# Optimization experiments

Hardware: AMD Instinct MI355X
Metric: run time of the kernel (lower is better)

## Reference

```python
import jax, jax.numpy as jnp
import numpy as np
from jax import lax

MAX_INT = 10000.0
V, T0, E, H = 100000, 20, 256, 256
T = T0 + 2          # tagset_size + 2 (start = T-2, stop = T-1)
B, S = 32, 512
H2 = H // 2


def setup_inputs() -> dict:
    key = jax.random.key(0)
    ks = jax.random.split(key, 18)
    sd = 0.08
    trans = jax.random.normal(ks[0], (T, T), jnp.float32)
    trans = trans.at[-2, :].set(-MAX_INT).at[:, -1].set(-MAX_INT)
    return {
        "X": jax.random.randint(ks[1], (B, S), 0, V, jnp.int64),
        "Y": jax.random.randint(ks[2], (B, S), 0, T0, jnp.int64),
        "emb": jax.random.normal(ks[3], (V, E), jnp.float32) * sd,
        "Wih_f": jax.random.normal(ks[4], (4 * H2, E), jnp.float32) * sd,
        "Whh_f": jax.random.normal(ks[5], (4 * H2, H2), jnp.float32) * sd,
        "bih_f": jax.random.normal(ks[6], (4 * H2,), jnp.float32) * sd,
        "bhh_f": jax.random.normal(ks[7], (4 * H2,), jnp.float32) * sd,
        "Wih_b": jax.random.normal(ks[8], (4 * H2, E), jnp.float32) * sd,
        "Whh_b": jax.random.normal(ks[9], (4 * H2, H2), jnp.float32) * sd,
        "bih_b": jax.random.normal(ks[10], (4 * H2,), jnp.float32) * sd,
        "bhh_b": jax.random.normal(ks[11], (4 * H2,), jnp.float32) * sd,
        "fcW": jax.random.normal(ks[12], (T, H), jnp.float32) * sd,
        "fcb": jax.random.normal(ks[13], (T,), jnp.float32) * sd,
        "trans": trans,
        # original draws random (h0, c0) of shape (2, seq_len, H//2) each call
        "h0": jax.random.normal(ks[14], (2, S, H2), jnp.float32),
        "c0": jax.random.normal(ks[15], (2, S, H2), jnp.float32),
    }


def _lstm_dir(x, h0, c0, Wih, Whh, bih, bhh, reverse):
    # x: [B, S, E]; scans over axis 0 (as torch LSTM with batch_first=False does here)
    def step(carry, xt):
        h, c = carry
        g = xt @ Wih.T + bih + h @ Whh.T + bhh          # [S, 4*H2]
        i, f, gg, o = jnp.split(g, 4, axis=-1)
        c2 = jax.nn.sigmoid(f) * c + jax.nn.sigmoid(i) * jnp.tanh(gg)
        h2 = jax.nn.sigmoid(o) * jnp.tanh(c2)
        return (h2, c2), h2
    xs = x[::-1] if reverse else x
    _, hs = lax.scan(step, (h0, c0), xs)
    return hs[::-1] if reverse else hs                  # [B, S, H2]


def _feats(X, emb, Wih_f, Whh_f, bih_f, bhh_f, Wih_b, Whh_b, bih_b, bhh_b,
           fcW, fcb, h0, c0):
    e = emb[X]                                           # [B, S, E]
    hf = _lstm_dir(e, h0[0], c0[0], Wih_f, Whh_f, bih_f, bhh_f, False)
    hb = _lstm_dir(e, h0[1], c0[1], Wih_b, Whh_b, bih_b, bhh_b, True)
    lstm_out = jnp.concatenate([hf, hb], axis=-1)        # [B, S, H]
    return lstm_out @ fcW.T + fcb                        # [B, S, T]


def _crf_loss(feats, Y, trans):
    # forward algorithm (log partition), vectorized over batch
    alpha0 = jnp.full((B, T), -MAX_INT, feats.dtype).at[:, -2].set(0.0)

    def step(alpha, feat_t):                             # feat_t: [B, T]
        # alpha_new[b, next] = LSE_prev(alpha[b,prev] + trans[next,prev]) + feat[b,next]
        new = jax.nn.logsumexp(alpha[:, None, :] + trans[None, :, :], axis=2) + feat_t
        return new, None

    alpha, _ = lax.scan(step, alpha0, jnp.swapaxes(feats, 0, 1))
    forward_score = jax.nn.logsumexp(alpha + trans[-1][None, :], axis=1).mean()

    # gold score
    start = jnp.full((B, 1), T - 2, Y.dtype)
    tags = jnp.concatenate([start, Y], axis=1)           # [B, S+1]
    emit = jnp.take_along_axis(feats, Y[..., None], axis=2)[..., 0].sum(axis=1)
    trans_sc = trans[tags[:, 1:], tags[:, :-1]].sum(axis=1) + trans[-1, tags[:, -1]]
    gold_score = (emit + trans_sc).mean()
    return forward_score - gold_score


def reference(X, Y, emb, Wih_f, Whh_f, bih_f, bhh_f, Wih_b, Whh_b, bih_b, bhh_b,
              fcW, fcb, trans, h0, c0):
    feats = _feats(X, emb, Wih_f, Whh_f, bih_f, bhh_f, Wih_b, Whh_b, bih_b, bhh_b,
                   fcW, fcb, h0, c0)
    score = _crf_loss(feats, Y, trans)
    return score, Y
```

## Files before the change

kernel.cpp:

```cpp
#include <hip/hip_runtime.h>
#include <hip/hip_bf16.h>
#include <stdint.h>

typedef __attribute__((ext_vector_type(8))) short short8;
typedef __attribute__((ext_vector_type(4))) float f32x4;
typedef __attribute__((ext_vector_type(4))) unsigned short ushort4v;
typedef __attribute__((ext_vector_type(4))) unsigned int uint4v;

#define NB 32
#define NS 512
#define NE 256
#define NH2 128
#define NG 512
#define NT 22

__device__ __forceinline__ unsigned short f2bf(float f) {
    union { float f; unsigned u; } v; v.f = f;
    unsigned r = v.u + 0x7fffu + ((v.u >> 16) & 1u);
    return (unsigned short)(r >> 16);
}
__device__ __forceinline__ float bf2f(unsigned short b) {
    union { unsigned u; float f; } v; v.u = ((unsigned)b) << 16;
    return v.f;
}
__device__ __forceinline__ unsigned cvt_pk_bf16(float a, float b) {
    unsigned r;
    asm("v_cvt_pk_bf16_f32 %0, %1, %2" : "=v"(r) : "v"(a), "v"(b));
    return r;
}
__device__ __forceinline__ void wg_barrier() {
    __builtin_amdgcn_sched_barrier(0);
    asm volatile("s_waitcnt lgkmcnt(0)" ::: "memory");
    __builtin_amdgcn_s_barrier();
    __builtin_amdgcn_sched_barrier(0);
}
#define GL16(gsrc, ldst)                                                              \
    __builtin_amdgcn_global_load_lds(                                                 \
        (const __attribute__((address_space(1))) unsigned int*)(gsrc),                \
        (__attribute__((address_space(3))) unsigned int*)(ldst), 16, 0, 0)

__global__ void k_pre(const int* X, const float* emb, const int* Y,
                      const float* Wih_f, const float* Wih_b,
                      const float* Whh_f, const float* Whh_b, const float* fcW,
                      unsigned short* ebf, unsigned short* Wb_ih,
                      unsigned short* Wb_hh, unsigned short* fcpad, float* out)
{
    int idx = blockIdx.x * blockDim.x + threadIdx.x;
    const int nEmb = NB * NS * 64;
    if (idx < nEmb) {
        int r = idx >> 6, lane = idx & 63;
        int xr = X[r];
        f32x4 v = *(const f32x4*)(emb + (size_t)xr * NE + lane * 4);
        ushort4v o;
        o[0] = f2bf(v[0]); o[1] = f2bf(v[1]); o[2] = f2bf(v[2]); o[3] = f2bf(v[3]);
        *(ushort4v*)(ebf + (size_t)r * NE + lane * 4) = o;
        return;
    }
    int j = idx - nEmb;
    const int n1 = 2 * NG * NE;
    const int n2 = 2 * NG * NH2;
    const int n3 = 2 * 32 * NH2;
    const int n4 = NB * NS;
    if (j < n1) {
        const float* src = (j < NG * NE) ? Wih_f : Wih_b;
        Wb_ih[j] = f2bf(src[j % (NG * NE)]);
    } else if (j < n1 + n2) {
        int i2 = j - n1;
        const float* src = (i2 < NG * NH2) ? Whh_f : Whh_b;
        Wb_hh[i2] = f2bf(src[i2 % (NG * NH2)]);
    } else if (j < n1 + n2 + n3) {
        int i3 = j - n1 - n2;
        int d = i3 / (32 * NH2);
        int jj = (i3 / NH2) % 32;
        int k = i3 % NH2;
        fcpad[i3] = (jj < NT) ? f2bf(fcW[jj * 256 + d * NH2 + k]) : (unsigned short)0;
    } else if (j < n1 + n2 + n3 + n4) {
        int i4 = j - n1 - n2 - n3;
        out[1 + i4] = (float)Y[i4];
    }
}

__launch_bounds__(256)
__global__ void k_xproj(const unsigned short* ebf, const unsigned short* Wb_ih,
                        const float* bih_f, const float* bhh_f,
                        const float* bih_b, const float* bhh_b,
                        unsigned short* Xp)
{
    __shared__ __align__(16) unsigned short Atile[2][128 * 64];
    __shared__ __align__(16) unsigned short Btile[2][128 * 64];
    int dir = blockIdx.z;
    int r0 = blockIdx.x * 128;
    int g0 = blockIdx.y * 128;
    int tid = threadIdx.x;
    int w = tid >> 6, lane = tid & 63;
    int wr = w >> 1, wc = w & 1;
    int lrow = lane & 15, kg = lane >> 4;
    int srow8 = lane >> 3, schunk = lane & 7;
    const float* bih = dir ? bih_b : bih_f;
    const float* bhh = dir ? bhh_b : bhh_f;
    const unsigned short* Bsrc = Wb_ih + ((size_t)dir * NG + g0) * NE;
    const unsigned short* Asrc = ebf + (size_t)r0 * NE;

#define STAGE(bufi, ks)                                                                \
    do {                                                                               \
        int k0_ = (ks) * 64;                                                           \
        _Pragma("unroll")                                                              \
        for (int i_ = 0; i_ < 4; ++i_) {                                               \
            int rr_ = (w * 4 + i_) * 8 + srow8;                                        \
            GL16(Asrc + (size_t)rr_ * NE + k0_ + schunk * 8, &Atile[bufi][(w * 4 + i_) * 512]); \
            GL16(Bsrc + (size_t)rr_ * NE + k0_ + schunk * 8, &Btile[bufi][(w * 4 + i_) * 512]); \
        }                                                                              \
    } while (0)

    STAGE(0, 0);
    f32x4 acc[4][4] = {};
#pragma unroll
    for (int ks = 0; ks < 4; ++ks) {
        const int cur = ks & 1;
        if (ks < 3) {
            STAGE(cur ^ 1, ks + 1);
            asm volatile("s_waitcnt vmcnt(8)" ::: "memory");
        } else {
            asm volatile("s_waitcnt vmcnt(0)" ::: "memory");
        }
        __builtin_amdgcn_sched_barrier(0);
        __builtin_amdgcn_s_barrier();
        __builtin_amdgcn_sched_barrier(0);
        short8 a[4][2], b[4][2];
#pragma unroll
        for (int mi = 0; mi < 4; ++mi)
#pragma unroll
            for (int kk = 0; kk < 2; ++kk)
                a[mi][kk] = *(const short8*)&Atile[cur][(wr * 64 + mi * 16 + lrow) * 64 + kk * 32 + kg * 8];
#pragma unroll
        for (int ni = 0; ni < 4; ++ni)
#pragma unroll
            for (int kk = 0; kk < 2; ++kk)
                b[ni][kk] = *(const short8*)&Btile[cur][(wc * 64 + ni * 16 + lrow) * 64 + kk * 32 + kg * 8];
#pragma unroll
        for (int mi = 0; mi < 4; ++mi)
#pragma unroll
            for (int ni = 0; ni < 4; ++ni)
#pragma unroll
                for (int kk = 0; kk < 2; ++kk)
                    acc[mi][ni] = __builtin_amdgcn_mfma_f32_16x16x32_bf16(a[mi][kk], b[ni][kk], acc[mi][ni], 0, 0, 0);
        asm volatile("s_waitcnt lgkmcnt(0)" ::: "memory");
        __builtin_amdgcn_sched_barrier(0);
        __builtin_amdgcn_s_barrier();
        __builtin_amdgcn_sched_barrier(0);
    }
#undef STAGE

#pragma unroll
    for (int ni = 0; ni < 4; ++ni) {
        int g = g0 + wc * 64 + ni * 16 + lrow;
        float bias = bih[g] + bhh[g];
#pragma unroll
        for (int mi = 0; mi < 4; ++mi) {
            int r = r0 + wr * 64 + mi * 16 + kg * 4;
            int t = r >> 9;
            int s = r & 511;
            int sb = s >> 4;
            unsigned short* dst = Xp + ((((size_t)dir * 32 + sb) * 32 + t) << 13) + g * 16 + (s & 15);
            unsigned o0 = f2bf(acc[mi][ni][0] + bias);
            unsigned o1 = f2bf(acc[mi][ni][1] + bias);
            unsigned o2 = f2bf(acc[mi][ni][2] + bias);
            unsigned o3 = f2bf(acc[mi][ni][3] + bias);
            uint2 pk; pk.x = o0 | (o1 << 16); pk.y = o2 | (o3 << 16);
            *(uint2*)dst = pk;
        }
    }
}

__launch_bounds__(512, 2)
__global__ void k_lstm(const unsigned short* Wb_hh, const unsigned short* fcpad,
                       const unsigned short* Xp, const float* h0, const float* c0,
                       unsigned short* featsP)
{
    __shared__ unsigned short h_lds[2][16 * 136];
    __shared__ unsigned short featsL[512 * 24];
    int dir = blockIdx.x >> 5;
    int sb = blockIdx.x & 31;
    int s0 = sb * 16;
    int tid = threadIdx.x;
    int w = tid >> 6, lane = tid & 63;
    int lrow = lane & 15, kg = lane >> 4;

    short8 bfr[4][4];
#pragma unroll
    for (int q = 0; q < 4; ++q) {
        const unsigned short* p = Wb_hh + ((size_t)dir * NG + (q * 128 + w * 16 + lrow)) * NH2 + kg * 8;
#pragma unroll
        for (int kf = 0; kf < 4; ++kf)
            bfr[q][kf] = *(const short8*)(p + kf * 32);
    }
    short8 fcfr[4];
    if (w < 2) {
        const unsigned short* p = fcpad + ((size_t)dir * 32 + (w * 16 + lrow)) * NH2 + kg * 8;
#pragma unroll
        for (int kf = 0; kf < 4; ++kf)
            fcfr[kf] = *(const short8*)(p + kf * 32);
    }

    float c[4], ho[4];
#pragma unroll
    for (int i = 0; i < 4; ++i)
        c[i] = c0[((size_t)dir * NS + s0 + kg * 4 + i) * NH2 + w * 16 + lrow];
    {
        int sl = tid >> 5, hq = tid & 31;
        f32x4 hv = *(const f32x4*)(h0 + ((size_t)dir * NS + s0 + sl) * NH2 + hq * 4);
        ushort4v hb; hb[0] = f2bf(hv[0]); hb[1] = f2bf(hv[1]); hb[2] = f2bf(hv[2]); hb[3] = f2bf(hv[3]);
        *(ushort4v*)&h_lds[0][sl * 136 + hq * 4] = hb;
    }

    const unsigned short* xbase = Xp + (((size_t)dir * 32 + sb) * 32) * 8192;
    int xoff0 = (w * 16 + lrow) * 16 + kg * 4;
    ushort4v xA[4], xB[4];
#pragma unroll
    for (int q = 0; q < 4; ++q)
        xA[q] = *(const ushort4v*)(xbase + (size_t)(dir ? 31 : 0) * 8192 + xoff0 + q * 2048);
#pragma unroll
    for (int q = 0; q < 4; ++q)
        xB[q] = *(const ushort4v*)(xbase + (size_t)(dir ? 30 : 1) * 8192 + xoff0 + q * 2048);
    __syncthreads();

#define LSTM_STEP(T, XV, PR, PW)                                                       \
    {                                                                                  \
        short8 afr[4];                                                                 \
        _Pragma("unroll")                                                              \
        for (int kf = 0; kf < 4; ++kf)                                                 \
            afr[kf] = *(const short8*)&h_lds[PR][lrow * 136 + kf * 32 + kg * 8];       \
        f32x4 accA[4], accB[4];                                                        \
        _Pragma("unroll")                                                              \
        for (int q = 0; q < 4; ++q) {                                                  \
            f32x4 ci_;                                                                 \
            ci_[0] = bf2f(XV[q][0]); ci_[1] = bf2f(XV[q][1]);                          \
            ci_[2] = bf2f(XV[q][2]); ci_[3] = bf2f(XV[q][3]);                          \
            accA[q] = __builtin_amdgcn_mfma_f32_16x16x32_bf16(afr[0], bfr[q][0], ci_, 0, 0, 0); \
            f32x4 z_ = {};                                                             \
            accB[q] = __builtin_amdgcn_mfma_f32_16x16x32_bf16(afr[2], bfr[q][2], z_, 0, 0, 0);  \
        }                                                                              \
        _Pragma("unroll")                                                              \
        for (int q = 0; q < 4; ++q) {                                                  \
            accA[q] = __builtin_amdgcn_mfma_f32_16x16x32_bf16(afr[1], bfr[q][1], accA[q], 0, 0, 0); \
            accB[q] = __builtin_amdgcn_mfma_f32_16x16x32_bf16(afr[3], bfr[q][3], accB[q], 0, 0, 0); \
        }                                                                              \
        if (w < 2 && (T) > 0) {                    \
            int txp_ = dir ? 32 - (T) : (T) - 1;                                       \
            f32x4 fa_ = {};                                                            \
            _Pragma("unroll")                                                          \
            for (int kf = 0; kf < 4; ++kf)                                             \
                fa_ = __builtin_amdgcn_mfma_f32_16x16x32_bf16(afr[kf], fcfr[kf], fa_, 0, 0, 0); \
            int tag_ = w * 16 + lrow;                                                  \
            if (tag_ < NT) {                                                           \
                unsigned r01_ = cvt_pk_bf16(fa_[0], fa_[1]);                           \
                unsigned r23_ = cvt_pk_bf16(fa_[2], fa_[3]);                           \
                int rb_ = (txp_ * 16 + kg * 4) * 24 + tag_;                            \
                featsL[rb_]      = (unsigned short)r01_;                               \
                featsL[rb_ + 24] = (unsigned short)(r01_ >> 16);                       \
                featsL[rb_ + 48] = (unsigned short)r23_;                               \
                featsL[rb_ + 72] = (unsigned short)(r23_ >> 16);                       \
            }                                                                          \
        }                                                                              \
        if ((T) + 2 < 32) {                                                            \
            int txn = dir ? 29 - (T) : (T) + 2;                                        \
            _Pragma("unroll")                                                          \
            for (int q = 0; q < 4; ++q)                                                \
                XV[q] = *(const ushort4v*)(xbase + (size_t)txn * 8192 + xoff0 + q * 2048); \
        }                                                                              \
        _Pragma("unroll")                                                              \
        for (int i = 0; i < 4; ++i) {                                                  \
            float gi_ = accA[0][i] + accB[0][i];                                       \
            float gf_ = accA[1][i] + accB[1][i];                                       \
            float gg_ = accA[2][i] + accB[2][i];                                       \
            float go_ = accA[3][i] + accB[3][i];                                       \
            float ef_ = __expf(-gf_);                                                  \
            float sfc_ = c[i] * __builtin_amdgcn_rcpf(1.f + ef_);                      \
            float eg2_ = __expf(2.f * gg_);                                            \
            float ei_ = __expf(-gi_);                                                  \
            float tgsi_ = (eg2_ - 1.f) * __builtin_amdgcn_rcpf((1.f + ei_) * (eg2_ + 1.f)); \
            float cn_ = sfc_ + tgsi_;                                                  \
            c[i] = cn_;                                                                \
            float ec2_ = __expf(2.f * cn_);                                            \
            float eo_ = __expf(-go_);                                                  \
            ho[i] = (ec2_ - 1.f) * __builtin_amdgcn_rcpf((1.f + eo_) * (ec2_ + 1.f));  \
        }                                                                              \
        {                                                                              \
            unsigned r01_ = cvt_pk_bf16(ho[0], ho[1]);                                 \
            unsigned r23_ = cvt_pk_bf16(ho[2], ho[3]);                                 \
            int hb_ = (kg * 4) * 136 + w * 16 + lrow;                                  \
            h_lds[PW][hb_]       = (unsigned short)r01_;                               \
            h_lds[PW][hb_ + 136] = (unsigned short)(r01_ >> 16);                       \
            h_lds[PW][hb_ + 272] = (unsigned short)r23_;                               \
            h_lds[PW][hb_ + 408] = (unsigned short)(r23_ >> 16);                       \
        }                                                                              \
        wg_barrier();                                                                  \
    }

    for (int tt = 0; tt < 16; ++tt) {
        LSTM_STEP(2 * tt,     xA, ((2 * tt) & 1),     (((2 * tt) & 1) ^ 1))
        LSTM_STEP(2 * tt + 1, xB, ((2 * tt + 1) & 1), (((2 * tt + 1) & 1) ^ 1))
    }
#undef LSTM_STEP

    if (w < 2) {
        short8 afr[4];
#pragma unroll
        for (int kf = 0; kf < 4; ++kf)
            afr[kf] = *(const short8*)&h_lds[0][lrow * 136 + kf * 32 + kg * 8];
        f32x4 fa = {};
#pragma unroll
        for (int kf = 0; kf < 4; ++kf)
            fa = __builtin_amdgcn_mfma_f32_16x16x32_bf16(afr[kf], fcfr[kf], fa, 0, 0, 0);
        int txl = dir ? 0 : 31;
        int tag = w * 16 + lrow;
        if (tag < NT) {
            unsigned r01 = cvt_pk_bf16(fa[0], fa[1]);
            unsigned r23 = cvt_pk_bf16(fa[2], fa[3]);
            int rb = (txl * 16 + kg * 4) * 24 + tag;
            featsL[rb]      = (unsigned short)r01;
            featsL[rb + 24] = (unsigned short)(r01 >> 16);
            featsL[rb + 48] = (unsigned short)r23;
            featsL[rb + 72] = (unsigned short)(r23 >> 16);
        }
    }
    __syncthreads();
    int ftx = tid >> 4, fs = tid & 15;
    unsigned short* gdst = featsP + (((size_t)dir * 32 + ftx) * 512 + s0 + fs) * 24;
    const unsigned short* lsrc = featsL + (ftx * 16 + fs) * 24;
#pragma unroll
    for (int j = 0; j < 3; ++j)
        ((uint4v*)gdst)[j] = ((const uint4v*)lsrc)[j];
}

__device__ __forceinline__ float mm_combine(const unsigned short* Rb, const unsigned short* Tb,
                                            int lane, f32x4 c[2][2])
{
    int lrow = lane & 15, kg = lane >> 4;
    short8 a0 = *(const short8*)(Rb + lrow * 32 + kg * 8);
    short8 a1 = *(const short8*)(Rb + (16 + lrow) * 32 + kg * 8);
    short8 b0 = *(const short8*)(Tb + lrow * 32 + kg * 8);
    short8 b1 = *(const short8*)(Tb + (16 + lrow) * 32 + kg * 8);
    c[0][0] = __builtin_amdgcn_mfma_f32_16x16x32_bf16(a0, b0, c[0][0], 0, 0, 0);
    c[0][1] = __builtin_amdgcn_mfma_f32_16x16x32_bf16(a0, b1, c[0][1], 0, 0, 0);
    c[1][0] = __builtin_amdgcn_mfma_f32_16x16x32_bf16(a1, b0, c[1][0], 0, 0, 0);
    c[1][1] = __builtin_amdgcn_mfma_f32_16x16x32_bf16(a1, b1, c[1][1], 0, 0, 0);
    float mx = 0.f;
#pragma unroll
    for (int ti = 0; ti < 2; ++ti)
#pragma unroll
        for (int tj = 0; tj < 2; ++tj)
#pragma unroll
            for (int i = 0; i < 4; ++i) mx = fmaxf(mx, c[ti][tj][i]);
#pragma unroll
    for (int off = 32; off; off >>= 1) mx = fmaxf(mx, __shfl_xor(mx, off));
    return fmaxf(mx, 1e-30f);
}

__device__ __forceinline__ void write_scaled(unsigned short* outp, bool Rlayout,
                                             int lane, const f32x4 c[2][2], float inv)
{
    int lrow = lane & 15, kg = lane >> 4;
    if (Rlayout) {
#pragma unroll
        for (int ti = 0; ti < 2; ++ti)
#pragma unroll
            for (int tj = 0; tj < 2; ++tj) {
                int cc = tj * 16 + lrow;
#pragma unroll
                for (int i = 0; i < 4; ++i) {
                    int r = ti * 16 + kg * 4 + i;
                    float v = (r < NT && cc < NT) ? c[ti][tj][i] * inv : 0.f;
                    outp[r * 32 + cc] = f2bf(v);
                }
            }
    } else {
#pragma unroll
        for (int ti = 0; ti < 2; ++ti)
#pragma unroll
            for (int tj = 0; tj < 2; ++tj) {
                int cc = tj * 16 + lrow;
                int r0 = ti * 16 + kg * 4;
                ushort4v pk;
#pragma unroll
                for (int i = 0; i < 4; ++i) {
                    int r = r0 + i;
                    float v = (r < NT && cc < NT) ? c[ti][tj][i] * inv : 0.f;
                    pk[i] = f2bf(v);
                }
                *(ushort4v*)(outp + cc * 32 + r0) = pk;
            }
    }
}

__launch_bounds__(256)
__global__ void k_fcrf(const unsigned short* featsP, const float* fcb, const float* trans,
                       const int* Y, unsigned short* Mseg, float* lscseg, float* goldp)
{
    __shared__ unsigned short mats[16 * 1024];
    __shared__ float etR[484], etT[484];
    __shared__ float ef[16 * 24];
    __shared__ float fl[16 * 24];
    __shared__ float lscm[16];
    int b = blockIdx.x, seg = blockIdx.y;
    int tid = threadIdx.x;
    int w = tid >> 6, lane = tid & 63;

    for (int i = tid; i < 484; i += 256) {
        float e = __expf(trans[i]);
        etR[i] = e;
        etT[(i % NT) * NT + (i / NT)] = e;
    }
    for (int i = tid; i < 16 * NT; i += 256) {
        int s = i / NT, j = i % NT;
        size_t base = ((size_t)b * 512 + seg * 16 + s) * 24 + j;
        float f = bf2f(featsP[base]) + bf2f(featsP[(size_t)32 * 512 * 24 + base]) + fcb[j];
        fl[s * 24 + j] = f;
        ef[s * 24 + j] = __expf(f);
    }
    if (tid < 16) lscm[tid] = 0.f;
    __syncthreads();

    if (w == 3 && lane < 16) {
        int sg = seg * 16 + lane;
        int y = Y[b * NS + sg];
        int yp = sg ? Y[b * NS + sg - 1] : (NT - 2);
        float gp = fl[lane * 24 + y] + trans[y * NT + yp];
#pragma unroll
        for (int off = 8; off; off >>= 1) gp += __shfl_xor(gp, off);
        if (lane == 0) goldp[b * 32 + seg] = gp;
    }

    for (int idx = tid; idx < 16 * 1024; idx += 256) {
        int t = idx >> 10, cell = idx & 1023, row = cell >> 5, col = cell & 31;
        float v = 0.f;
        if (row < NT && col < NT) {
            v = (t & 1) ? etR[row * NT + col] * ef[t * 24 + row]
                        : etT[row * NT + col] * ef[t * 24 + col];
        }
        mats[idx] = f2bf(v);
    }
    __syncthreads();

    for (int lvl = 0; lvl < 4; ++lvl) {
        int nP = 8 >> lvl;
        for (int p = w; p < nP; p += 4) {
            int aslot = (2 * p) << lvl, bslot = (2 * p + 1) << lvl;
            f32x4 c[2][2] = {};
            float mx = mm_combine(mats + bslot * 1024, mats + aslot * 1024, lane, c);
            float inv = __builtin_amdgcn_rcpf(mx);
            float nlsc = lscm[aslot] + lscm[bslot] + __logf(mx);
            if (lvl < 3) {
                write_scaled(mats + aslot * 1024, (p & 1) != 0, lane, c, inv);
                if (lane == 0) lscm[aslot] = nlsc;
            } else {
                write_scaled(Mseg + ((size_t)b * 32 + seg) * 1024, (seg & 1) != 0, lane, c, inv);
                if (lane == 0) lscseg[b * 32 + seg] = nlsc;
            }
        }
        __syncthreads();
    }
}

__launch_bounds__(256)
__global__ void k_crf2(const unsigned short* Mseg, const float* lscseg,
                       const float* trans, const int* Y, const float* goldp,
                       float* fwd_sc, float* gold_sc)
{
    __shared__ unsigned short mats[16 * 1024];
    __shared__ float lscm[16];
    __shared__ float tl[484];
    __shared__ float col20[32];
    int b = blockIdx.x;
    int tid = threadIdx.x;
    int w = tid >> 6, lane = tid & 63;
    int lrow = lane & 15, kg = lane >> 4;

    for (int i = tid; i < 484; i += 256) tl[i] = trans[i];
    __syncthreads();

    const unsigned short* base = Mseg + (size_t)b * 32 * 1024;
    for (int p = w; p < 16; p += 4) {
        f32x4 c[2][2] = {};
        float mx = mm_combine(base + (2 * p + 1) * 1024, base + (2 * p) * 1024, lane, c);
        float inv = __builtin_amdgcn_rcpf(mx);
        float nlsc = lscseg[b * 32 + 2 * p] + lscseg[b * 32 + 2 * p + 1] + __logf(mx);
        write_scaled(mats + p * 1024, (p & 1) != 0, lane, c, inv);
        if (lane == 0) lscm[p] = nlsc;
    }
    __syncthreads();

    for (int lvl = 0; lvl < 4; ++lvl) {
        int nP = 8 >> lvl;
        for (int p = w; p < nP; p += 4) {
            int aslot = (2 * p) << lvl, bslot = (2 * p + 1) << lvl;
            f32x4 c[2][2] = {};
            float mx = mm_combine(mats + bslot * 1024, mats + aslot * 1024, lane, c);
            if (lvl < 3) {
                float inv = __builtin_amdgcn_rcpf(mx);
                float nlsc = lscm[aslot] + lscm[bslot] + __logf(mx);
                write_scaled(mats + aslot * 1024, (p & 1) != 0, lane, c, inv);
                if (lane == 0) lscm[aslot] = nlsc;
            } else {
                if (lrow == 4) {
#pragma unroll
                    for (int ti = 0; ti < 2; ++ti)
#pragma unroll
                        for (int i = 0; i < 4; ++i)
                            col20[ti * 16 + kg * 4 + i] = c[ti][1][i];
                }
                if (lane == 0) lscm[0] = lscm[0] + lscm[8];
            }
        }
        __syncthreads();
    }

    if (w == 0) {
        float v = 0.f;
        if (lane < NT) v = __expf(tl[(NT - 1) * NT + lane]) * col20[lane];
#pragma unroll
        for (int off = 32; off; off >>= 1) v += __shfl_xor(v, off);
        if (lane == 0) fwd_sc[b] = __logf(v) + lscm[0];
    }
    if (w == 1) {
        float g = (lane < 32) ? goldp[b * 32 + lane] : 0.f;
#pragma unroll
        for (int off = 16; off; off >>= 1) g += __shfl_xor(g, off);
        if (lane == 0) gold_sc[b] = g + tl[(NT - 1) * NT + Y[b * NS + NS - 1]];
    }
}

__global__ void k_final(const float* fwd_sc, const float* gold_sc, float* out)
{
    float v = (threadIdx.x < NB) ? (fwd_sc[threadIdx.x] - gold_sc[threadIdx.x]) : 0.f;
#pragma unroll
    for (int off = 32; off; off >>= 1) v += __shfl_xor(v, off);
    if (threadIdx.x == 0) out[0] = v * (1.f / NB);
}

extern "C" void kernel_launch(void* const* d_in, const int* in_sizes, int n_in,
                              void* d_out, int out_size, void* d_ws, size_t ws_size,
                              hipStream_t stream)
{
    const int* X = (const int*)d_in[0];
    const int* Y = (const int*)d_in[1];
    const float* emb = (const float*)d_in[2];
    const float* Wih_f = (const float*)d_in[3];
    const float* Whh_f = (const float*)d_in[4];
    const float* bih_f = (const float*)d_in[5];
    const float* bhh_f = (const float*)d_in[6];
    const float* Wih_b = (const float*)d_in[7];
    const float* Whh_b = (const float*)d_in[8];
    const float* bih_b = (const float*)d_in[9];
    const float* bhh_b = (const float*)d_in[10];
    const float* fcW = (const float*)d_in[11];
    const float* fcb = (const float*)d_in[12];
    const float* trans = (const float*)d_in[13];
    const float* h0 = (const float*)d_in[14];
    const float* c0 = (const float*)d_in[15];
    float* out = (float*)d_out;

    char* ws = (char*)d_ws;
    unsigned short* Wb_ih  = (unsigned short*)(ws + 0);
    unsigned short* Wb_hh  = (unsigned short*)(ws + 524288);
    unsigned short* fcpad  = (unsigned short*)(ws + 786432);
    unsigned short* Xp     = (unsigned short*)(ws + 802816);
    unsigned short* featsP = (unsigned short*)(ws + 34357248);
    float* goldp           = (float*)(ws + 35930112);
    float* fwd_sc          = (float*)(ws + 35934208);
    float* gold_sc         = (float*)(ws + 35934336);
    unsigned short* ebf    = (unsigned short*)(ws + 35934464);
    unsigned short* Mseg   = ebf;
    float* lscseg          = (float*)(ws + 44323072);

    k_pre<<<dim3(5728), dim3(256), 0, stream>>>(X, emb, Y, Wih_f, Wih_b, Whh_f, Whh_b,
                                                fcW, ebf, Wb_ih, Wb_hh, fcpad, out);
    k_xproj<<<dim3(128, 4, 2), dim3(256), 0, stream>>>(ebf, Wb_ih, bih_f, bhh_f, bih_b, bhh_b, Xp);
    k_lstm<<<dim3(64), dim3(512), 0, stream>>>(Wb_hh, fcpad, Xp, h0, c0, featsP);
    k_fcrf<<<dim3(32, 32), dim3(256), 0, stream>>>(featsP, fcb, trans, Y, Mseg, lscseg, goldp);
    k_crf2<<<dim3(NB), dim3(256), 0, stream>>>(Mseg, lscseg, trans, Y, goldp, fwd_sc, gold_sc);
    k_final<<<dim3(1), dim3(64), 0, stream>>>(fwd_sc, gold_sc, out);
    (void)in_sizes; (void)n_in; (void)out_size; (void)ws_size;
}
```

Before: 94.23 us.

## Merge LSTM directions per block, fold final reduction into CRF kernel

The LSTM kernel now runs both directions in one block (32 blocks instead of 64), interleaving two independent recurrences between barriers to hide latency and halve the barrier count. Feature outputs go straight to global memory instead of being staged in LDS. The separate final-reduction launch is removed; the last k_crf2 block, found through an atomic counter, computes the mean. The k_fcrf matrix fill also writes packed bf16 pairs. Costs: double the register use for weights (launch_bounds 2 may spill), half the CUs busy, and scattered 2-byte global stores.

After: 134.2 us. 42.4% more time.

```diff
diff --git a/kernel.cpp b/kernel.cpp
--- a/kernel.cpp
+++ b/kernel.cpp
@@ -43,9 +43,11 @@
                       const float* Wih_f, const float* Wih_b,
                       const float* Whh_f, const float* Whh_b, const float* fcW,
                       unsigned short* ebf, unsigned short* Wb_ih,
-                      unsigned short* Wb_hh, unsigned short* fcpad, float* out)
+                      unsigned short* Wb_hh, unsigned short* fcpad, float* out,
+                      unsigned* done_cnt)
 {
     int idx = blockIdx.x * blockDim.x + threadIdx.x;
+    if (idx == 0) *done_cnt = 0;
     const int nEmb = NB * NS * 64;
     if (idx < nEmb) {
         int r = idx >> 6, lane = idx & 63;
@@ -177,96 +179,106 @@
                        const unsigned short* Xp, const float* h0, const float* c0,
                        unsigned short* featsP)
 {
-    __shared__ unsigned short h_lds[2][16 * 136];
-    __shared__ unsigned short featsL[512 * 24];
-    int dir = blockIdx.x >> 5;
-    int sb = blockIdx.x & 31;
+    __shared__ unsigned short h_lds0[2][16 * 136];
+    __shared__ unsigned short h_lds1[2][16 * 136];
+    int sb = blockIdx.x;
     int s0 = sb * 16;
     int tid = threadIdx.x;
     int w = tid >> 6, lane = tid & 63;
     int lrow = lane & 15, kg = lane >> 4;
 
-    short8 bfr[4][4];
+    short8 bfr0[4][4], bfr1[4][4];
 #pragma unroll
     for (int q = 0; q < 4; ++q) {
-        const unsigned short* p = Wb_hh + ((size_t)dir * NG + (q * 128 + w * 16 + lrow)) * NH2 + kg * 8;
-#pragma unroll
-        for (int kf = 0; kf < 4; ++kf)
-            bfr[q][kf] = *(const short8*)(p + kf * 32);
+        const unsigned short* p0 = Wb_hh + ((size_t)(q * 128 + w * 16 + lrow)) * NH2 + kg * 8;
+        const unsigned short* p1 = p0 + (size_t)NG * NH2;
+#pragma unroll
+        for (int kf = 0; kf < 4; ++kf) {
+            bfr0[q][kf] = *(const short8*)(p0 + kf * 32);
+            bfr1[q][kf] = *(const short8*)(p1 + kf * 32);
+        }
     }
     short8 fcfr[4];
-    if (w < 2) {
-        const unsigned short* p = fcpad + ((size_t)dir * 32 + (w * 16 + lrow)) * NH2 + kg * 8;
+    if (w < 4) {
+        int fd = (w >> 1);
+        int ft = (w & 1);
+        fd = (w < 2) ? 0 : 1;
+        ft = (w < 2) ? w : (w - 2);
+        const unsigned short* p = fcpad + ((size_t)fd * 32 + (ft * 16 + lrow)) * NH2 + kg * 8;
 #pragma unroll
         for (int kf = 0; kf < 4; ++kf)
             fcfr[kf] = *(const short8*)(p + kf * 32);
     }
 
-    float c[4], ho[4];
-#pragma unroll
-    for (int i = 0; i < 4; ++i)
-        c[i] = c0[((size_t)dir * NS + s0 + kg * 4 + i) * NH2 + w * 16 + lrow];
+    float c0s[4], c1s[4], ho[4];
+#pragma unroll
+    for (int i = 0; i < 4; ++i) {
+        c0s[i] = c0[((size_t)(s0 + kg * 4 + i)) * NH2 + w * 16 + lrow];
+        c1s[i] = c0[((size_t)(NS + s0 + kg * 4 + i)) * NH2 + w * 16 + lrow];
+    }
     {
         int sl = tid >> 5, hq = tid & 31;
-        f32x4 hv = *(const f32x4*)(h0 + ((size_t)dir * NS + s0 + sl) * NH2 + hq * 4);
-        ushort4v hb; hb[0] = f2bf(hv[0]); hb[1] = f2bf(hv[1]); hb[2] = f2bf(hv[2]); hb[3] = f2bf(hv[3]);
-        *(ushort4v*)&h_lds[0][sl * 136 + hq * 4] = hb;
-    }
-
-    const unsigned short* xbase = Xp + (((size_t)dir * 32 + sb) * 32) * 8192;
+        f32x4 hv0 = *(const f32x4*)(h0 + ((size_t)(s0 + sl)) * NH2 + hq * 4);
+        f32x4 hv1 = *(const f32x4*)(h0 + ((size_t)(NS + s0 + sl)) * NH2 + hq * 4);
+        ushort4v hb0, hb1;
+#pragma unroll
+        for (int i = 0; i < 4; ++i) { hb0[i] = f2bf(hv0[i]); hb1[i] = f2bf(hv1[i]); }
+        *(ushort4v*)&h_lds0[0][sl * 136 + hq * 4] = hb0;
+        *(ushort4v*)&h_lds1[0][sl * 136 + hq * 4] = hb1;
+    }
+
+    const unsigned short* xbase0 = Xp + ((size_t)sb * 32) * 8192;
+    const unsigned short* xbase1 = Xp + ((size_t)(32 + sb) * 32) * 8192;
     int xoff0 = (w * 16 + lrow) * 16 + kg * 4;
-    ushort4v xA[4], xB[4];
-#pragma unroll
-    for (int q = 0; q < 4; ++q)
-        xA[q] = *(const ushort4v*)(xbase + (size_t)(dir ? 31 : 0) * 8192 + xoff0 + q * 2048);
-#pragma unroll
-    for (int q = 0; q < 4; ++q)
-        xB[q] = *(const ushort4v*)(xbase + (size_t)(dir ? 30 : 1) * 8192 + xoff0 + q * 2048);
+    ushort4v x0A[4], x0B[4], x1A[4], x1B[4];
+#pragma unroll
+    for (int q = 0; q < 4; ++q) {
+        x0A[q] = *(const ushort4v*)(xbase0 + (size_t)0 * 8192 + xoff0 + q * 2048);
+        x0B[q] = *(const ushort4v*)(xbase0 + (size_t)1 * 8192 + xoff0 + q * 2048);
+        x1A[q] = *(const ushort4v*)(xbase1 + (size_t)31 * 8192 + xoff0 + q * 2048);
+        x1B[q] = *(const ushort4v*)(xbase1 + (size_t)30 * 8192 + xoff0 + q * 2048);
+    }
     __syncthreads();
 
-#define LSTM_STEP(T, XV, PR, PW)                                                       \
+#define LSTM_CH(T, XV, PR, PW, D, HL, CST, XB)                                         \
     {                                                                                  \
         short8 afr[4];                                                                 \
         _Pragma("unroll")                                                              \
         for (int kf = 0; kf < 4; ++kf)                                                 \
-            afr[kf] = *(const short8*)&h_lds[PR][lrow * 136 + kf * 32 + kg * 8];       \
+            afr[kf] = *(const short8*)&HL[PR][lrow * 136 + kf * 32 + kg * 8];          \
         f32x4 accA[4], accB[4];                                                        \
         _Pragma("unroll")                                                              \
         for (int q = 0; q < 4; ++q) {                                                  \
             f32x4 ci_;                                                                 \
             ci_[0] = bf2f(XV[q][0]); ci_[1] = bf2f(XV[q][1]);                          \
             ci_[2] = bf2f(XV[q][2]); ci_[3] = bf2f(XV[q][3]);                          \
-            accA[q] = __builtin_amdgcn_mfma_f32_16x16x32_bf16(afr[0], bfr[q][0], ci_, 0, 0, 0); \
+            accA[q] = __builtin_amdgcn_mfma_f32_16x16x32_bf16(afr[0], bfr##D[q][0], ci_, 0, 0, 0); \
             f32x4 z_ = {};                                                             \
-            accB[q] = __builtin_amdgcn_mfma_f32_16x16x32_bf16(afr[2], bfr[q][2], z_, 0, 0, 0);  \
+            accB[q] = __builtin_amdgcn_mfma_f32_16x16x32_bf16(afr[2], bfr##D[q][2], z_, 0, 0, 0);  \
         }                                                                              \
         _Pragma("unroll")                                                              \
         for (int q = 0; q < 4; ++q) {                                                  \
-            accA[q] = __builtin_amdgcn_mfma_f32_16x16x32_bf16(afr[1], bfr[q][1], accA[q], 0, 0, 0); \
-            accB[q] = __builtin_amdgcn_mfma_f32_16x16x32_bf16(afr[3], bfr[q][3], accB[q], 0, 0, 0); \
+            accA[q] = __builtin_amdgcn_mfma_f32_16x16x32_bf16(afr[1], bfr##D[q][1], accA[q], 0, 0, 0); \
+            accB[q] = __builtin_amdgcn_mfma_f32_16x16x32_bf16(afr[3], bfr##D[q][3], accB[q], 0, 0, 0); \
         }                                                                              \
-        if (w < 2 && (T) > 0) {                    \
-            int txp_ = dir ? 32 - (T) : (T) - 1;                                       \
+        if ((D == 0 ? (w < 2) : (w == 2 || w == 3)) && (T) > 0) {                      \
+            int txp_ = D ? 32 - (T) : (T) - 1;                                         \
             f32x4 fa_ = {};                                                            \
             _Pragma("unroll")                                                          \
             for (int kf = 0; kf < 4; ++kf)                                             \
                 fa_ = __builtin_amdgcn_mfma_f32_16x16x32_bf16(afr[kf], fcfr[kf], fa_, 0, 0, 0); \
-            int tag_ = w * 16 + lrow;                                                  \
+            int tag_ = (D == 0 ? w : (w - 2)) * 16 + lrow;                             \
             if (tag_ < NT) {                                                           \
-                unsigned r01_ = cvt_pk_bf16(fa_[0], fa_[1]);                           \
-                unsigned r23_ = cvt_pk_bf16(fa_[2], fa_[3]);                           \
-                int rb_ = (txp_ * 16 + kg * 4) * 24 + tag_;                            \
-                featsL[rb_]      = (unsigned short)r01_;                               \
-                featsL[rb_ + 24] = (unsigned short)(r01_ >> 16);                       \
-                featsL[rb_ + 48] = (unsigned short)r23_;                               \
-                featsL[rb_ + 72] = (unsigned short)(r23_ >> 16);                       \
+                _Pragma("unroll")                                                      \
+                for (int i = 0; i < 4; ++i)                                            \
+                    featsP[(((size_t)D * 32 + txp_) * 512 + s0 + kg * 4 + i) * 24 + tag_] = f2bf(fa_[i]); \
             }                                                                          \
         }                                                                              \
         if ((T) + 2 < 32) {                                                            \
-            int txn = dir ? 29 - (T) : (T) + 2;                                        \
+            int txn_ = D ? 29 - (T) : (T) + 2;                                         \
             _Pragma("unroll")                                                          \
             for (int q = 0; q < 4; ++q)                                                \
-                XV[q] = *(const ushort4v*)(xbase + (size_t)txn * 8192 + xoff0 + q * 2048); \
+                XV[q] = *(const ushort4v*)(XB + (size_t)txn_ * 8192 + xoff0 + q * 2048); \
         }                                                                              \
         _Pragma("unroll")                                                              \
         for (int i = 0; i < 4; ++i) {                                                  \
@@ -275,12 +287,12 @@
             float gg_ = accA[2][i] + accB[2][i];                                       \
             float go_ = accA[3][i] + accB[3][i];                                       \
             float ef_ = __expf(-gf_);                                                  \
-            float sfc_ = c[i] * __builtin_amdgcn_rcpf(1.f + ef_);                      \
+            float sfc_ = CST[i] * __builtin_amdgcn_rcpf(1.f + ef_);                    \
             float eg2_ = __expf(2.f * gg_);                                            \
             float ei_ = __expf(-gi_);                                                  \
             float tgsi_ = (eg2_ - 1.f) * __builtin_amdgcn_rcpf((1.f + ei_) * (eg2_ + 1.f)); \
             float cn_ = sfc_ + tgsi_;                                                  \
-            c[i] = cn_;                                                                \
+            CST[i] = cn_;                                                              \
             float ec2_ = __expf(2.f * cn_);                                            \
             float eo_ = __expf(-go_);                                                  \
             ho[i] = (ec2_ - 1.f) * __builtin_amdgcn_rcpf((1.f + eo_) * (ec2_ + 1.f));  \
@@ -289,48 +301,44 @@
             unsigned r01_ = cvt_pk_bf16(ho[0], ho[1]);                                 \
             unsigned r23_ = cvt_pk_bf16(ho[2], ho[3]);                                 \
             int hb_ = (kg * 4) * 136 + w * 16 + lrow;                                  \
-            h_lds[PW][hb_]       = (unsigned short)r01_;                               \
-            h_lds[PW][hb_ + 136] = (unsigned short)(r01_ >> 16);                       \
-            h_lds[PW][hb_ + 272] = (unsigned short)r23_;                               \
-            h_lds[PW][hb_ + 408] = (unsigned short)(r23_ >> 16);                       \
+            HL[PW][hb_]       = (unsigned short)r01_;                                  \
+            HL[PW][hb_ + 136] = (unsigned short)(r01_ >> 16);                          \
+            HL[PW][hb_ + 272] = (unsigned short)r23_;                                  \
+            HL[PW][hb_ + 408] = (unsigned short)(r23_ >> 16);                          \
         }                                                                              \
-        wg_barrier();                                                                  \
-    }
+    }
+
+#define LSTM_STEP2(T, XV0, XV1, PR, PW)                                                \
+    LSTM_CH(T, XV0, PR, PW, 0, h_lds0, c0s, xbase0)                                    \
+    LSTM_CH(T, XV1, PR, PW, 1, h_lds1, c1s, xbase1)                                    \
+    wg_barrier();
 
     for (int tt = 0; tt < 16; ++tt) {
-        LSTM_STEP(2 * tt,     xA, ((2 * tt) & 1),     (((2 * tt) & 1) ^ 1))
-        LSTM_STEP(2 * tt + 1, xB, ((2 * tt + 1) & 1), (((2 * tt + 1) & 1) ^ 1))
-    }
-#undef LSTM_STEP
-
-    if (w < 2) {
+        LSTM_STEP2(2 * tt,     x0A, x1A, ((2 * tt) & 1),     (((2 * tt) & 1) ^ 1))
+        LSTM_STEP2(2 * tt + 1, x0B, x1B, ((2 * tt + 1) & 1), (((2 * tt + 1) & 1) ^ 1))
+    }
+#undef LSTM_STEP2
+#undef LSTM_CH
+
+    if (w < 4) {
+        const unsigned short* hl = (w < 2) ? &h_lds0[0][0] : &h_lds1[0][0];
         short8 afr[4];
 #pragma unroll
         for (int kf = 0; kf < 4; ++kf)
-            afr[kf] = *(const short8*)&h_lds[0][lrow * 136 + kf * 32 + kg * 8];
+            afr[kf] = *(const short8*)&hl[lrow * 136 + kf * 32 + kg * 8];
         f32x4 fa = {};
 #pragma unroll
         for (int kf = 0; kf < 4; ++kf)
             fa = __builtin_amdgcn_mfma_f32_16x16x32_bf16(afr[kf], fcfr[kf], fa, 0, 0, 0);
-        int txl = dir ? 0 : 31;
-        int tag = w * 16 + lrow;
+        int d = (w < 2) ? 0 : 1;
+        int txl = d ? 0 : 31;
+        int tag = ((w < 2) ? w : (w - 2)) * 16 + lrow;
         if (tag < NT) {
-            unsigned r01 = cvt_pk_bf16(fa[0], fa[1]);
-            unsigned r23 = cvt_pk_bf16(fa[2], fa[3]);
-            int rb = (txl * 16 + kg * 4) * 24 + tag;
-            featsL[rb]      = (unsigned short)r01;
-            featsL[rb + 24] = (unsigned short)(r01 >> 16);
-            featsL[rb + 48] = (unsigned short)r23;
-            featsL[rb + 72] = (unsigned short)(r23 >> 16);
+#pragma unroll
+            for (int i = 0; i < 4; ++i)
+                featsP[(((size_t)d * 32 + txl) * 512 + s0 + kg * 4 + i) * 24 + tag] = f2bf(fa[i]);
         }
     }
-    __syncthreads();
-    int ftx = tid >> 4, fs = tid & 15;
-    unsigned short* gdst = featsP + (((size_t)dir * 32 + ftx) * 512 + s0 + fs) * 24;
-    const unsigned short* lsrc = featsL + (ftx * 16 + fs) * 24;
-#pragma unroll
-    for (int j = 0; j < 3; ++j)
-        ((uint4v*)gdst)[j] = ((const uint4v*)lsrc)[j];
 }
 
 __device__ __forceinline__ float mm_combine(const unsigned short* Rb, const unsigned short* Tb,
@@ -431,14 +439,19 @@
         if (lane == 0) goldp[b * 32 + seg] = gp;
     }
 
-    for (int idx = tid; idx < 16 * 1024; idx += 256) {
-        int t = idx >> 10, cell = idx & 1023, row = cell >> 5, col = cell & 31;
-        float v = 0.f;
-        if (row < NT && col < NT) {
-            v = (t & 1) ? etR[row * NT + col] * ef[t * 24 + row]
-                        : etT[row * NT + col] * ef[t * 24 + col];
+    for (int u = tid; u < 16 * 512; u += 256) {
+        int t = u >> 9, cell2 = u & 511, row = cell2 >> 4, col = (cell2 & 15) * 2;
+        float v0 = 0.f, v1 = 0.f;
+        if (row < NT) {
+            if (t & 1) {
+                if (col < NT)     v0 = etR[row * NT + col]     * ef[t * 24 + row];
+                if (col + 1 < NT) v1 = etR[row * NT + col + 1] * ef[t * 24 + row];
+            } else {
+                if (col < NT)     v0 = etT[row * NT + col]     * ef[t * 24 + col];
+                if (col + 1 < NT) v1 = etT[row * NT + col + 1] * ef[t * 24 + col + 1];
+            }
         }
-        mats[idx] = f2bf(v);
+        ((unsigned*)mats)[u] = (unsigned)f2bf(v0) | ((unsigned)f2bf(v1) << 16);
     }
     __syncthreads();
 
@@ -465,12 +478,13 @@
 __launch_bounds__(256)
 __global__ void k_crf2(const unsigned short* Mseg, const float* lscseg,
                        const float* trans, const int* Y, const float* goldp,
-                       float* fwd_sc, float* gold_sc)
+                       float* fwd_sc, float* gold_sc, unsigned* done_cnt, float* out)
 {
     __shared__ unsigned short mats[16 * 1024];
     __shared__ float lscm[16];
     __shared__ float tl[484];
     __shared__ float col20[32];
+    __shared__ unsigned lastflag;
     int b = blockIdx.x;
     int tid = threadIdx.x;
     int w = tid >> 6, lane = tid & 63;
@@ -528,14 +542,19 @@
         for (int off = 16; off; off >>= 1) g += __shfl_xor(g, off);
         if (lane == 0) gold_sc[b] = g + tl[(NT - 1) * NT + Y[b * NS + NS - 1]];
     }
-}
-
-__global__ void k_final(const float* fwd_sc, const float* gold_sc, float* out)
-{
-    float v = (threadIdx.x < NB) ? (fwd_sc[threadIdx.x] - gold_sc[threadIdx.x]) : 0.f;
-#pragma unroll
-    for (int off = 32; off; off >>= 1) v += __shfl_xor(v, off);
-    if (threadIdx.x == 0) out[0] = v * (1.f / NB);
+    __syncthreads();
+    if (tid == 0) {
+        __threadfence();
+        lastflag = (atomicAdd(done_cnt, 1u) == 31u) ? 1u : 0u;
+    }
+    __syncthreads();
+    if (lastflag && w == 0) {
+        __threadfence();
+        float v = (lane < NB) ? (fwd_sc[lane] - gold_sc[lane]) : 0.f;
+#pragma unroll
+        for (int off = 32; off; off >>= 1) v += __shfl_xor(v, off);
+        if (lane == 0) out[0] = v * (1.f / NB);
+    }
 }
 
 extern "C" void kernel_launch(void* const* d_in, const int* in_sizes, int n_in,
@@ -569,16 +588,17 @@
     float* goldp           = (float*)(ws + 35930112);
     float* fwd_sc          = (float*)(ws + 35934208);
     float* gold_sc         = (float*)(ws + 35934336);
-    unsigned short* ebf    = (unsigned short*)(ws + 35934464);
+    unsigned* done_cnt     = (unsigned*)(ws + 35934464);
+    unsigned short* ebf    = (unsigned short*)(ws + 35934592);
     unsigned short* Mseg   = ebf;
-    float* lscseg          = (float*)(ws + 44323072);
+    float* lscseg          = (float*)(ws + 44323200);
 
     k_pre<<<dim3(5728), dim3(256), 0, stream>>>(X, emb, Y, Wih_f, Wih_b, Whh_f, Whh_b,
-                                                fcW, ebf, Wb_ih, Wb_hh, fcpad, out);
+                                                fcW, ebf, Wb_ih, Wb_hh, fcpad, out, done_cnt);
     k_xproj<<<dim3(128, 4, 2), dim3(256), 0, stream>>>(ebf, Wb_ih, bih_f, bhh_f, bih_b, bhh_b, Xp);
-    k_lstm<<<dim3(64), dim3(512), 0, stream>>>(Wb_hh, fcpad, Xp, h0, c0, featsP);
+    k_lstm<<<dim3(32), dim3(512), 0, stream>>>(Wb_hh, fcpad, Xp, h0, c0, featsP);
     k_fcrf<<<dim3(32, 32), dim3(256), 0, stream>>>(featsP, fcb, trans, Y, Mseg, lscseg, goldp);
-    k_crf2<<<dim3(NB), dim3(256), 0, stream>>>(Mseg, lscseg, trans, Y, goldp, fwd_sc, gold_sc);
-    k_final<<<dim3(1), dim3(64), 0, stream>>>(fwd_sc, gold_sc, out);
+    k_crf2<<<dim3(NB), dim3(256), 0, stream>>>(Mseg, lscseg, trans, Y, goldp,
+                                               fwd_sc, gold_sc, done_cnt, out);
     (void)in_sizes; (void)n_in; (void)out_size; (void)ws_size;
 }
```
